# Performance work log

Hardware: AMD Instinct MI355X
Metric: run time of the kernel (lower is better)

The kernel has to match this reference:

```python
import jax, jax.numpy as jnp
import numpy as np

NUM_DIMS = 256  # from init_kwargs; scale = 1/sqrt(num_dims)
SCALE = 1.0 / np.float32(np.sqrt(NUM_DIMS))


def setup_inputs() -> dict:
    key = jax.random.key(0)
    kq, kk, kv = jax.random.split(key, 3)
    B, C, N = 8, 256, 2048
    q = jax.random.normal(kq, (B, C, N), dtype=jnp.float32)
    k = jax.random.normal(kk, (B, C, N), dtype=jnp.float32)
    v = jax.random.normal(kv, (B, C, N), dtype=jnp.float32)
    return {"q": q, "k": k, "v": v}


def reference(q, k, v):
    # NCH format: q,k,v are [B, C, N]
    # logits[b,i,j] = sum_c k[b,c,i] * q[b,c,j], scaled
    logits = jnp.einsum('bci,bcj->bij', k, q) * SCALE
    # torch.softmax(..., dim=1): normalize over key index i for each query j
    weights = jax.nn.softmax(logits, axis=1)  # [B, N, N]
    # out[b,c,j] = sum_i v[b,c,i] * weights[b,i,j]
    out = jnp.einsum('bci,bij->bcj', v, weights)  # [B, C, N]
    return (out, weights)
```

## Files before the change

kernel.cpp:

```cpp
#include <hip/hip_runtime.h>
#include <math.h>

#define BATCH 8
#define CDIM 256
#define NDIM 2048
#define SCALE 0.0625f

typedef _Float16 half8v __attribute__((ext_vector_type(8)));
typedef _Float16 half4v __attribute__((ext_vector_type(4)));
typedef float floatx4 __attribute__((ext_vector_type(4)));

#define WS_SPART 0
#define WS_KT    1048576
#define WS_QT    (1048576 + 8388608)
#define WS_EHT   (1048576 + 2 * 8388608)

#define BSWZ(c, j) (((((c) + (j) + ((j) >> 3)) & 7)) << 3)

__global__ __launch_bounds__(256) void prep_kernel(const float* __restrict__ Q,
                                                   const float* __restrict__ K,
                                                   _Float16* __restrict__ Kt,
                                                   _Float16* __restrict__ Qt) {
    const int g = blockIdx.x * 256 + threadIdx.x;
    const float* src = (blockIdx.y == 0) ? K : Q;
    _Float16* dst = (blockIdx.y == 0) ? Kt : Qt;
    const int b = g >> 15, r = g & 32767;
    const int iq = r & 511, cq = r >> 9;
    const float* p = src + (size_t)b * CDIM * NDIM + (size_t)(cq * 4) * NDIM + iq * 4;
    float fr[4][4];
    *(float4*)fr[0] = *(const float4*)(p);
    *(float4*)fr[1] = *(const float4*)(p + NDIM);
    *(float4*)fr[2] = *(const float4*)(p + 2 * NDIM);
    *(float4*)fr[3] = *(const float4*)(p + 3 * NDIM);
    const int cb = cq >> 3, cc0 = (cq & 7) * 4;
#pragma unroll
    for (int ii = 0; ii < 4; ++ii) {
        const int i = iq * 4 + ii;
        const int ib = i >> 7, il = i & 127;
        half4v h = {(_Float16)fr[0][ii], (_Float16)fr[1][ii],
                    (_Float16)fr[2][ii], (_Float16)fr[3][ii]};
        *(half4v*)&dst[((((size_t)(b * 16 + ib) * 8 + cb) * 128 + il) * 32) + cc0] = h;
    }
}

__global__ __launch_bounds__(256) void gemm1_kernel(const _Float16* __restrict__ Kt,
                                                    const _Float16* __restrict__ Qt,
                                                    _Float16* __restrict__ EhT,
                                                    float* __restrict__ Spart) {
    __shared__ _Float16 Al[128 * 40];
    __shared__ _Float16 Bl[128 * 40];
    __shared__ _Float16 LT[128 * 128];
    __shared__ float Sl[2][128];
    const int b = blockIdx.z, ib2 = blockIdx.y, jb2 = blockIdx.x;
    const _Float16* Ab = Kt + (size_t)(b * 16 + ib2) * 8 * 4096;
    const _Float16* Bb = Qt + (size_t)(b * 16 + jb2) * 8 * 4096;
    const int t = threadIdx.x, wave = t >> 6, lane = t & 63;
    const int wy = wave >> 1, wx = wave & 1, quad = lane >> 4, lr = lane & 15;
    floatx4 acc[4][4] = {};
    const int ci0 = t * 2, ci1 = t * 2 + 1;
    _Float16* wA0 = &Al[(ci0 >> 2) * 40 + (ci0 & 3) * 8];
    _Float16* wA1 = &Al[(ci1 >> 2) * 40 + (ci1 & 3) * 8];
    _Float16* wB0 = &Bl[(ci0 >> 2) * 40 + (ci0 & 3) * 8];
    _Float16* wB1 = &Bl[(ci1 >> 2) * 40 + (ci1 & 3) * 8];

    for (int cb = 0; cb < 8; ++cb) {
        half8v a0 = *(const half8v*)(Ab + cb * 4096 + ci0 * 8);
        half8v a1 = *(const half8v*)(Ab + cb * 4096 + ci1 * 8);
        half8v b0 = *(const half8v*)(Bb + cb * 4096 + ci0 * 8);
        half8v b1 = *(const half8v*)(Bb + cb * 4096 + ci1 * 8);
        __syncthreads();
        *(half8v*)wA0 = a0; *(half8v*)wA1 = a1;
        *(half8v*)wB0 = b0; *(half8v*)wB1 = b1;
        __syncthreads();
        half8v af[4], bf[4];
#pragma unroll
        for (int m = 0; m < 4; ++m)
            af[m] = *(const half8v*)&Al[(wy * 64 + m * 16 + lr) * 40 + quad * 8];
#pragma unroll
        for (int n = 0; n < 4; ++n)
            bf[n] = *(const half8v*)&Bl[(wx * 64 + n * 16 + lr) * 40 + quad * 8];
#pragma unroll
        for (int m = 0; m < 4; ++m)
#pragma unroll
            for (int n = 0; n < 4; ++n)
                acc[m][n] = __builtin_amdgcn_mfma_f32_16x16x32_f16(af[m], bf[n], acc[m][n], 0, 0, 0);
    }

    float psum[4] = {0.f, 0.f, 0.f, 0.f};
#pragma unroll
    for (int m = 0; m < 4; ++m) {
#pragma unroll
        for (int n = 0; n < 4; ++n) {
            const int j_loc = wx * 64 + n * 16 + lr;
#pragma unroll
            for (int r = 0; r < 4; ++r) {
                const int i_loc = wy * 64 + m * 16 + quad * 4 + r;
                float e = __expf(acc[m][n][r] * SCALE);
                psum[n] += e;
                LT[j_loc * 128 + (((i_loc >> 3) ^ (j_loc & 7)) << 3) + (i_loc & 7)] = (_Float16)e;
            }
        }
    }
#pragma unroll
    for (int n = 0; n < 4; ++n) {
        float s = psum[n];
        s += __shfl_xor(s, 16, 64);
        s += __shfl_xor(s, 32, 64);
        if (quad == 0) Sl[wy][wx * 64 + n * 16 + lr] = s;
    }
    __syncthreads();
    if (t < 128)
        Spart[((size_t)(b * 16 + ib2)) * 2048 + jb2 * 128 + t] = Sl[0][t] + Sl[1][t];

    const int jh = wave >> 1, ih = wave & 1;
    _Float16* dst = EhT + ((size_t)((b * 32 + jb2 * 2 + jh) * 32) + ib2 * 2 + ih) * 4096;
#pragma unroll
    for (int cc = 0; cc < 8; ++cc) {
        const int j = jh * 64 + cc * 8 + (lane >> 3);
        half8v h = *(const half8v*)&LT[j * 128 + (((ih * 8 + (lane & 7)) ^ (lane >> 3)) << 3)];
        *(half8v*)&dst[cc * 512 + lane * 8] = h;
    }
}

__global__ __launch_bounds__(256) void gemm2_kernel(const float* __restrict__ V,
                                                    const _Float16* __restrict__ EhT,
                                                    const float* __restrict__ Spart,
                                                    float* __restrict__ W,
                                                    float* __restrict__ Out) {
    __shared__ _Float16 As[128 * 72];
    __shared__ _Float16 Bs[128 * 72];
    __shared__ float invSl[128];
    const int b = blockIdx.z, cc2 = blockIdx.y, jb2 = blockIdx.x;
    const int t = threadIdx.x, wave = t >> 6, lane = t & 63;
    const int wy = wave >> 1, wx = wave & 1, quad = lane >> 4, lr = lane & 15;
    const float* Vb = V + ((size_t)(b * 256 + cc2 * 128)) * 2048;
    floatx4 acc[4][4] = {};

    if (t < 128) {
        float s = 0.f;
#pragma unroll
        for (int p = 0; p < 16; ++p)
            s += Spart[((size_t)(b * 16 + p)) * 2048 + jb2 * 128 + t];
        invSl[t] = 1.0f / s;
    }
    __syncthreads();

    const int tj4 = t & 31, ti8 = t >> 5, j0 = tj4 * 4;
    const float4 ivW = make_float4(invSl[j0], invSl[j0 + 1], invSl[j0 + 2], invSl[j0 + 3]);
    float* Wb = W + ((size_t)b * 2048) * 2048 + jb2 * 128;

    for (int it = 0; it < 32; ++it) {
        float4 av[8];
#pragma unroll
        for (int u = 0; u < 8; ++u) {
            const int f = u * 256 + t;
            const int c = f >> 4, i4 = f & 15;
            av[u] = *(const float4*)&Vb[(size_t)c * 2048 + it * 64 + i4 * 4];
        }
        half8v bv[4];
#pragma unroll
        for (int u = 0; u < 4; ++u) {
            const int f = u * 256 + t;
            const int jl = f >> 3, c8 = f & 7;
            const int jb = jb2 * 2 + (jl >> 6);
            bv[u] = *(const half8v*)&EhT[((size_t)((b * 32 + jb) * 32) + it) * 4096 +
                                         (jl & 63) * 64 + c8 * 8];
        }
        __syncthreads();
#pragma unroll
        for (int u = 0; u < 8; ++u) {
            const int f = u * 256 + t;
            const int c = f >> 4, i4 = f & 15;
            half4v h = {(_Float16)av[u].x, (_Float16)av[u].y,
                        (_Float16)av[u].z, (_Float16)av[u].w};
            *(half4v*)&As[c * 72 + i4 * 4] = h;
        }
#pragma unroll
        for (int u = 0; u < 4; ++u) {
            const int f = u * 256 + t;
            const int jl = f >> 3, c8 = f & 7;
            *(half8v*)&Bs[jl * 72 + BSWZ(c8, jl)] = bv[u];
        }
        __syncthreads();
#pragma unroll
        for (int ks = 0; ks < 2; ++ks) {
            half8v af[4], bf[4];
#pragma unroll
            for (int m = 0; m < 4; ++m)
                af[m] = *(const half8v*)&As[(wy * 64 + m * 16 + lr) * 72 + ks * 32 + quad * 8];
#pragma unroll
            for (int n = 0; n < 4; ++n) {
                const int row = wx * 64 + n * 16 + lr;
                bf[n] = *(const half8v*)&Bs[row * 72 + BSWZ(ks * 4 + quad, row)];
            }
#pragma unroll
            for (int m = 0; m < 4; ++m)
#pragma unroll
                for (int n = 0; n < 4; ++n)
                    acc[m][n] = __builtin_amdgcn_mfma_f32_16x16x32_f16(af[m], bf[n], acc[m][n], 0, 0, 0);
        }
        if ((it & 1) == cc2) {
            half8v hvr[4];
#pragma unroll
            for (int r = 0; r < 4; ++r) {
                const int j = j0 + r;
                hvr[r] = *(const half8v*)&Bs[j * 72 + BSWZ(ti8, j)];
            }
            float* Wr = Wb + (size_t)(it * 64 + ti8 * 8) * 2048;
#pragma unroll
            for (int e = 0; e < 8; ++e) {
                float4 o = make_float4((float)hvr[0][e] * ivW.x,
                                       (float)hvr[1][e] * ivW.y,
                                       (float)hvr[2][e] * ivW.z,
                                       (float)hvr[3][e] * ivW.w);
                *(float4*)&Wr[(size_t)e * 2048 + j0] = o;
            }
        }
    }

    float* Ob = Out + ((size_t)(b * 256 + cc2 * 128)) * 2048 + jb2 * 128;
    float iv[4];
#pragma unroll
    for (int n = 0; n < 4; ++n)
        iv[n] = invSl[wx * 64 + n * 16 + lr];
#pragma unroll
    for (int m = 0; m < 4; ++m) {
        const int c0r = wy * 64 + m * 16 + quad * 4;
#pragma unroll
        for (int n = 0; n < 4; ++n) {
            const int j = wx * 64 + n * 16 + lr;
#pragma unroll
            for (int r = 0; r < 4; ++r)
                Ob[(size_t)(c0r + r) * 2048 + j] = acc[m][n][r] * iv[n];
        }
    }
}

extern "C" void kernel_launch(void* const* d_in, const int* in_sizes, int n_in,
                              void* d_out, int out_size, void* d_ws, size_t ws_size,
                              hipStream_t stream) {
    const float* q = (const float*)d_in[0];
    const float* k = (const float*)d_in[1];
    const float* v = (const float*)d_in[2];
    float* out = (float*)d_out;
    float* w = out + (size_t)BATCH * CDIM * NDIM;

    char* ws = (char*)d_ws;
    float* Spart = (float*)(ws + WS_SPART);
    _Float16* Kt = (_Float16*)(ws + WS_KT);
    _Float16* Qt = (_Float16*)(ws + WS_QT);
    _Float16* EhT = (_Float16*)(ws + WS_EHT);

    prep_kernel<<<dim3(1024, 2), 256, 0, stream>>>(q, k, Kt, Qt);
    gemm1_kernel<<<dim3(16, 16, 8), 256, 0, stream>>>(Kt, Qt, EhT, Spart);
    gemm2_kernel<<<dim3(16, 2, 8), 256, 0, stream>>>(v, EhT, Spart, w, out);
}
```

Measured before the change: 299.9 us.

## Pre-convert V to fp16 and double-buffer gemm2 global loads with 512 threads

V is converted to fp16 in the prep kernel, so gemm2 reads half the bytes and skips in-loop conversion. gemm2 now runs 8 waves per block with a 4x2 tile per wave, and it prefetches the next iteration's V and E tiles into registers while computing the current one. The A tile in LDS is now swizzled as well. The cost is an extra fp16 copy of V written to and read from workspace, plus more register pressure from the double buffers.

Measured after the change: 274.1 us. 8.6% less time.

```diff
diff --git a/kernel.cpp b/kernel.cpp
--- a/kernel.cpp
+++ b/kernel.cpp
@@ -12,15 +12,29 @@
 
 #define WS_SPART 0
 #define WS_KT    1048576
-#define WS_QT    (1048576 + 8388608)
-#define WS_EHT   (1048576 + 2 * 8388608)
+#define WS_QT    9437184
+#define WS_VT    17825792
+#define WS_EHT   26214400
 
 #define BSWZ(c, j) (((((c) + (j) + ((j) >> 3)) & 7)) << 3)
 
 __global__ __launch_bounds__(256) void prep_kernel(const float* __restrict__ Q,
                                                    const float* __restrict__ K,
+                                                   const float* __restrict__ V,
                                                    _Float16* __restrict__ Kt,
-                                                   _Float16* __restrict__ Qt) {
+                                                   _Float16* __restrict__ Qt,
+                                                   _Float16* __restrict__ Vt) {
+    if (blockIdx.y == 2) {
+        const int t = threadIdx.x;
+#pragma unroll
+        for (int u = 0; u < 4; ++u) {
+            const size_t idx = (size_t)blockIdx.x * 4096 + (u * 256 + t) * 4;
+            float4 f = *(const float4*)&V[idx];
+            half4v h = {(_Float16)f.x, (_Float16)f.y, (_Float16)f.z, (_Float16)f.w};
+            *(half4v*)&Vt[idx] = h;
+        }
+        return;
+    }
     const int g = blockIdx.x * 256 + threadIdx.x;
     const float* src = (blockIdx.y == 0) ? K : Q;
     _Float16* dst = (blockIdx.y == 0) ? Kt : Qt;
@@ -122,7 +136,65 @@
     }
 }
 
-__global__ __launch_bounds__(256) void gemm2_kernel(const float* __restrict__ V,
+#define G2_LOAD(IT, AV, BV)                                                        \
+    do {                                                                           \
+        _Pragma("unroll") for (int u = 0; u < 2; ++u) {                            \
+            const int f = u * 512 + t;                                             \
+            const int c = f >> 3, i8 = f & 7;                                      \
+            AV[u] = *(const half8v*)&Vtb[(size_t)c * 2048 + (IT) * 64 + i8 * 8];   \
+        }                                                                          \
+        _Pragma("unroll") for (int u = 0; u < 2; ++u) {                            \
+            const int f = u * 512 + t;                                             \
+            const int jl = f >> 3, c8 = f & 7;                                     \
+            const int jbv = jb2 * 2 + (jl >> 6);                                   \
+            BV[u] = *(const half8v*)&EhT[((size_t)((b * 32 + jbv) * 32) + (IT)) *  \
+                                             4096 +                                \
+                                         (jl & 63) * 64 + c8 * 8];                 \
+        }                                                                          \
+    } while (0)
+
+#define G2_STEP(IT, AVc, BVc, ITN, AVn, BVn, DUTY)                                 \
+    do {                                                                           \
+        __syncthreads();                                                           \
+        _Pragma("unroll") for (int u = 0; u < 2; ++u) {                            \
+            const int f = u * 512 + t;                                             \
+            const int c = f >> 3, i8 = f & 7;                                      \
+            *(half8v*)&As[c * 72 + BSWZ(i8, c)] = AVc[u];                          \
+        }                                                                          \
+        _Pragma("unroll") for (int u = 0; u < 2; ++u) {                            \
+            const int f = u * 512 + t;                                             \
+            const int jl = f >> 3, c8 = f & 7;                                     \
+            *(half8v*)&Bs[jl * 72 + BSWZ(c8, jl)] = BVc[u];                        \
+        }                                                                          \
+        __syncthreads();                                                           \
+        G2_LOAD(ITN, AVn, BVn);                                                    \
+        _Pragma("unroll") for (int ks = 0; ks < 2; ++ks) {                         \
+            half8v af[4], bf[2];                                                   \
+            _Pragma("unroll") for (int m = 0; m < 4; ++m) {                        \
+                const int row = wy * 64 + m * 16 + lr;                             \
+                af[m] = *(const half8v*)&As[row * 72 + BSWZ(ks * 4 + quad, row)];  \
+            }                                                                      \
+            _Pragma("unroll") for (int n = 0; n < 2; ++n) {                        \
+                const int row = wx * 32 + n * 16 + lr;                             \
+                bf[n] = *(const half8v*)&Bs[row * 72 + BSWZ(ks * 4 + quad, row)];  \
+            }                                                                      \
+            _Pragma("unroll") for (int m = 0; m < 4; ++m)                          \
+                _Pragma("unroll") for (int n = 0; n < 2; ++n)                      \
+                    acc[m][n] = __builtin_amdgcn_mfma_f32_16x16x32_f16(            \
+                        af[m], bf[n], acc[m][n], 0, 0, 0);                         \
+        }                                                                          \
+        if (DUTY) {                                                                \
+            half8v hv0 = *(const half8v*)&Bs[j0 * 72 + BSWZ(ti, j0)];              \
+            half8v hv1 = *(const half8v*)&Bs[(j0 + 1) * 72 + BSWZ(ti, j0 + 1)];    \
+            float* Wr = Wb + (size_t)((IT) * 64 + ti * 8) * 2048;                  \
+            _Pragma("unroll") for (int e = 0; e < 8; ++e) {                        \
+                float2 o = make_float2((float)hv0[e] * iv0, (float)hv1[e] * iv1);  \
+                *(float2*)&Wr[(size_t)e * 2048 + j0] = o;                          \
+            }                                                                      \
+        }                                                                          \
+    } while (0)
+
+__global__ __launch_bounds__(512) void gemm2_kernel(const _Float16* __restrict__ Vt,
                                                     const _Float16* __restrict__ EhT,
                                                     const float* __restrict__ Spart,
                                                     float* __restrict__ W,
@@ -132,9 +204,9 @@
     __shared__ float invSl[128];
     const int b = blockIdx.z, cc2 = blockIdx.y, jb2 = blockIdx.x;
     const int t = threadIdx.x, wave = t >> 6, lane = t & 63;
-    const int wy = wave >> 1, wx = wave & 1, quad = lane >> 4, lr = lane & 15;
-    const float* Vb = V + ((size_t)(b * 256 + cc2 * 128)) * 2048;
-    floatx4 acc[4][4] = {};
+    const int wy = wave >> 2, wx = wave & 3, quad = lane >> 4, lr = lane & 15;
+    const _Float16* Vtb = Vt + ((size_t)(b * 256 + cc2 * 128)) * 2048;
+    floatx4 acc[4][2] = {};
 
     if (t < 128) {
         float s = 0.f;
@@ -145,90 +217,30 @@
     }
     __syncthreads();
 
-    const int tj4 = t & 31, ti8 = t >> 5, j0 = tj4 * 4;
-    const float4 ivW = make_float4(invSl[j0], invSl[j0 + 1], invSl[j0 + 2], invSl[j0 + 3]);
+    const int j0 = (t & 63) * 2, ti = t >> 6;
+    const float iv0 = invSl[j0], iv1 = invSl[j0 + 1];
     float* Wb = W + ((size_t)b * 2048) * 2048 + jb2 * 128;
 
-    for (int it = 0; it < 32; ++it) {
-        float4 av[8];
-#pragma unroll
-        for (int u = 0; u < 8; ++u) {
-            const int f = u * 256 + t;
-            const int c = f >> 4, i4 = f & 15;
-            av[u] = *(const float4*)&Vb[(size_t)c * 2048 + it * 64 + i4 * 4];
-        }
-        half8v bv[4];
-#pragma unroll
-        for (int u = 0; u < 4; ++u) {
-            const int f = u * 256 + t;
-            const int jl = f >> 3, c8 = f & 7;
-            const int jb = jb2 * 2 + (jl >> 6);
-            bv[u] = *(const half8v*)&EhT[((size_t)((b * 32 + jb) * 32) + it) * 4096 +
-                                         (jl & 63) * 64 + c8 * 8];
-        }
-        __syncthreads();
-#pragma unroll
-        for (int u = 0; u < 8; ++u) {
-            const int f = u * 256 + t;
-            const int c = f >> 4, i4 = f & 15;
-            half4v h = {(_Float16)av[u].x, (_Float16)av[u].y,
-                        (_Float16)av[u].z, (_Float16)av[u].w};
-            *(half4v*)&As[c * 72 + i4 * 4] = h;
-        }
-#pragma unroll
-        for (int u = 0; u < 4; ++u) {
-            const int f = u * 256 + t;
-            const int jl = f >> 3, c8 = f & 7;
-            *(half8v*)&Bs[jl * 72 + BSWZ(c8, jl)] = bv[u];
-        }
-        __syncthreads();
-#pragma unroll
-        for (int ks = 0; ks < 2; ++ks) {
-            half8v af[4], bf[4];
-#pragma unroll
-            for (int m = 0; m < 4; ++m)
-                af[m] = *(const half8v*)&As[(wy * 64 + m * 16 + lr) * 72 + ks * 32 + quad * 8];
-#pragma unroll
-            for (int n = 0; n < 4; ++n) {
-                const int row = wx * 64 + n * 16 + lr;
-                bf[n] = *(const half8v*)&Bs[row * 72 + BSWZ(ks * 4 + quad, row)];
-            }
-#pragma unroll
-            for (int m = 0; m < 4; ++m)
-#pragma unroll
-                for (int n = 0; n < 4; ++n)
-                    acc[m][n] = __builtin_amdgcn_mfma_f32_16x16x32_f16(af[m], bf[n], acc[m][n], 0, 0, 0);
-        }
-        if ((it & 1) == cc2) {
-            half8v hvr[4];
-#pragma unroll
-            for (int r = 0; r < 4; ++r) {
-                const int j = j0 + r;
-                hvr[r] = *(const half8v*)&Bs[j * 72 + BSWZ(ti8, j)];
-            }
-            float* Wr = Wb + (size_t)(it * 64 + ti8 * 8) * 2048;
-#pragma unroll
-            for (int e = 0; e < 8; ++e) {
-                float4 o = make_float4((float)hvr[0][e] * ivW.x,
-                                       (float)hvr[1][e] * ivW.y,
-                                       (float)hvr[2][e] * ivW.z,
-                                       (float)hvr[3][e] * ivW.w);
-                *(float4*)&Wr[(size_t)e * 2048 + j0] = o;
-            }
-        }
+    half8v av0[2], bv0[2], av1[2], bv1[2];
+    G2_LOAD(0, av0, bv0);
+    const bool dutyE = (cc2 == 0), dutyO = (cc2 == 1);
+    for (int ip = 0; ip < 16; ++ip) {
+        const int itE = ip * 2, itO = ip * 2 + 1;
+        G2_STEP(itE, av0, bv0, itO, av1, bv1, dutyE);
+        G2_STEP(itO, av1, bv1, (itO + 1) & 31, av0, bv0, dutyO);
     }
 
     float* Ob = Out + ((size_t)(b * 256 + cc2 * 128)) * 2048 + jb2 * 128;
-    float iv[4];
-#pragma unroll
-    for (int n = 0; n < 4; ++n)
-        iv[n] = invSl[wx * 64 + n * 16 + lr];
+    float iv[2];
+#pragma unroll
+    for (int n = 0; n < 2; ++n)
+        iv[n] = invSl[wx * 32 + n * 16 + lr];
 #pragma unroll
     for (int m = 0; m < 4; ++m) {
         const int c0r = wy * 64 + m * 16 + quad * 4;
 #pragma unroll
-        for (int n = 0; n < 4; ++n) {
-            const int j = wx * 64 + n * 16 + lr;
+        for (int n = 0; n < 2; ++n) {
+            const int j = wx * 32 + n * 16 + lr;
 #pragma unroll
             for (int r = 0; r < 4; ++r)
                 Ob[(size_t)(c0r + r) * 2048 + j] = acc[m][n][r] * iv[n];
@@ -249,9 +261,10 @@
     float* Spart = (float*)(ws + WS_SPART);
     _Float16* Kt = (_Float16*)(ws + WS_KT);
     _Float16* Qt = (_Float16*)(ws + WS_QT);
+    _Float16* Vt = (_Float16*)(ws + WS_VT);
     _Float16* EhT = (_Float16*)(ws + WS_EHT);
 
-    prep_kernel<<<dim3(1024, 2), 256, 0, stream>>>(q, k, Kt, Qt);
+    prep_kernel<<<dim3(1024, 3), 256, 0, stream>>>(q, k, v, Kt, Qt, Vt);
     gemm1_kernel<<<dim3(16, 16, 8), 256, 0, stream>>>(Kt, Qt, EhT, Spart);
-    gemm2_kernel<<<dim3(16, 2, 8), 256, 0, stream>>>(v, EhT, Spart, w, out);
-}
+    gemm2_kernel<<<dim3(16, 2, 8), 512, 0, stream>>>(Vt, EhT, Spart, w, out);
+}
```
